# Performance work log

Hardware: AMD Instinct MI355X
Metric: run time of the kernel (lower is better)

## Reference

```python
import jax, jax.numpy as jnp
import numpy as np

B, T, D_IN = 8, 1024, 320
L, H, DK, DV, DM, DI = 6, 8, 64, 64, 512, 2048


def _pe_table():
    pos = np.arange(T, dtype=np.float32)[:, None]
    div = np.exp(np.arange(0, DM, 2, dtype=np.float32) * (-np.log(10000.0) / DM))
    pe = np.zeros((T, DM), np.float32)
    pe[:, 0::2] = np.sin(pos * div)
    pe[:, 1::2] = np.cos(pos * div)
    return jnp.asarray(pe)


def setup_inputs() -> dict:
    key = jax.random.key(0)
    ks = jax.random.split(key, 16)
    rn = lambda k, shape, std: (jax.random.normal(k, shape, jnp.float32) * std)
    inp = {}
    inp["padded_input"] = jax.random.normal(ks[0], (B, T, D_IN), jnp.float32)
    inp["input_lengths"] = jax.random.randint(ks[1], (B,), T // 2, T + 1)
    # input projection + input layernorm (weights stored as [in, out])
    inp["w_in"] = rn(ks[2], (D_IN, DM), 0.02)
    inp["b_in"] = jnp.zeros((DM,), jnp.float32)
    inp["ln_in_g"] = jnp.ones((DM,), jnp.float32)
    inp["ln_in_b"] = jnp.zeros((DM,), jnp.float32)
    inp["pe"] = _pe_table()
    # stacked per-layer params, leading dim L
    inp["wq"] = rn(ks[3], (L, DM, H * DK), np.sqrt(2.0 / (DM + DK)))
    inp["bq"] = jnp.zeros((L, H * DK), jnp.float32)
    inp["wk"] = rn(ks[4], (L, DM, H * DK), np.sqrt(2.0 / (DM + DK)))
    inp["bk"] = jnp.zeros((L, H * DK), jnp.float32)
    inp["wv"] = rn(ks[5], (L, DM, H * DV), np.sqrt(2.0 / (DM + DV)))
    inp["bv"] = jnp.zeros((L, H * DV), jnp.float32)
    inp["wfc"] = rn(ks[6], (L, H * DV, DM), np.sqrt(2.0 / (H * DV + DM)))
    inp["bfc"] = jnp.zeros((L, DM), jnp.float32)
    inp["ln1_g"] = jnp.ones((L, DM), jnp.float32)
    inp["ln1_b"] = jnp.zeros((L, DM), jnp.float32)
    inp["w1"] = rn(ks[7], (L, DM, DI), np.sqrt(2.0 / (DM + DI)))
    inp["b1"] = jnp.zeros((L, DI), jnp.float32)
    inp["w2"] = rn(ks[8], (L, DI, DM), np.sqrt(2.0 / (DM + DI)))
    inp["b2"] = jnp.zeros((L, DM), jnp.float32)
    inp["ln2_g"] = jnp.ones((L, DM), jnp.float32)
    inp["ln2_b"] = jnp.zeros((L, DM), jnp.float32)
    return inp


def _layer_norm(x, g, b):
    mu = jnp.mean(x, axis=-1, keepdims=True)
    var = jnp.var(x, axis=-1, keepdims=True)
    return (x - mu) * jax.lax.rsqrt(var + 1e-5) * g + b


def _encoder(padded_input, input_lengths, w_in, b_in, ln_in_g, ln_in_b, pe,
             wq, bq, wk, bk, wv, bv, wfc, bfc, ln1_g, ln1_b,
             w1, b1, w2, b2, ln2_g, ln2_b):
    pos = jnp.arange(T)
    key_pad = pos[None, :] >= input_lengths[:, None]          # [B,T] True at pad
    non_pad = (~key_pad).astype(padded_input.dtype)[:, :, None]  # [B,T,1]
    scale = 1.0 / jnp.sqrt(jnp.float32(DK))

    x = _layer_norm(padded_input @ w_in + b_in, ln_in_g, ln_in_b) + pe[None]

    def body(x, p):
        Wq, Bq, Wk, Bk, Wv, Bv, Wfc, Bfc, G1, Bn1, W1, Bf1, W2, Bf2, G2, Bn2 = p
        res = x
        q = (x @ Wq + Bq).reshape(B, T, H, DK)
        k = (x @ Wk + Bk).reshape(B, T, H, DK)
        v = (x @ Wv + Bv).reshape(B, T, H, DV)
        attn = jnp.einsum('bqhd,bkhd->bhqk', q, k) * scale
        attn = jnp.where(key_pad[:, None, None, :], -jnp.inf, attn)
        attn = jax.nn.softmax(attn, axis=-1)
        o = jnp.einsum('bhqk,bkhd->bqhd', attn, v).reshape(B, T, H * DV)
        x = _layer_norm(o @ Wfc + Bfc + res, G1, Bn1) * non_pad
        res = x
        h = jax.nn.relu(x @ W1 + Bf1)
        x = _layer_norm(h @ W2 + Bf2 + res, G2, Bn2) * non_pad
        return x, None

    x, _ = jax.lax.scan(body, x, (wq, bq, wk, bk, wv, bv, wfc, bfc,
                                  ln1_g, ln1_b, w1, b1, w2, b2, ln2_g, ln2_b))
    return x


def reference(padded_input, input_lengths, w_in, b_in, ln_in_g, ln_in_b, pe,
              wq, bq, wk, bk, wv, bv, wfc, bfc, ln1_g, ln1_b,
              w1, b1, w2, b2, ln2_g, ln2_b):
    # dropout is identity in eval mode
    return _encoder(padded_input, input_lengths, w_in, b_in, ln_in_g, ln_in_b, pe,
                    wq, bq, wk, bk, wv, bv, wfc, bfc, ln1_g, ln1_b,
                    w1, b1, w2, b2, ln2_g, ln2_b)
```

## Files before the change

### kernel.cpp

```cpp
#include <hip/hip_runtime.h>
#include <hip/hip_bf16.h>


typedef unsigned short bh16;
typedef __bf16 bf16x8 __attribute__((ext_vector_type(8)));
typedef float f32x4 __attribute__((ext_vector_type(4)));
typedef unsigned int u32x4 __attribute__((ext_vector_type(4)));
typedef unsigned int u32x2 __attribute__((ext_vector_type(2)));

#define DEVI static __device__ __forceinline__

DEVI bh16 f2bf(float f) {
  union { float f; unsigned u; } x; x.f = f;
  unsigned r = x.u + 0x7fffu + ((x.u >> 16) & 1u);
  return (bh16)(r >> 16);
}
DEVI float bf2f(bh16 u) {
  union { unsigned u; float f; } x; x.u = ((unsigned)u) << 16; return x.f;
}
DEVI bf16x8 ld16(const bh16* p) {
  return __builtin_bit_cast(bf16x8, *(const u32x4*)p);
}
DEVI bf16x8 ld16b(const char* p) {
  return __builtin_bit_cast(bf16x8, *(const u32x4*)p);
}
DEVI f32x4 mfma16(bf16x8 a, bf16x8 b, f32x4 c) {
  return __builtin_amdgcn_mfma_f32_16x16x32_bf16(a, b, c, 0, 0, 0);
}
DEVI void async16(const void* g, void* l) {
  __builtin_amdgcn_global_load_lds(
      (const __attribute__((address_space(1))) void*)g,
      (__attribute__((address_space(3))) void*)l, 16, 0, 0);
}

__global__ __launch_bounds__(256) void tcvt(
    const float* __restrict__ in, bh16* __restrict__ out,
    int K, int N, long long inLS, long long outLS, int rowOff) {
  int l = blockIdx.z;
  in += (size_t)l * inLS;
  out += (size_t)l * outLS + (size_t)rowOff * K;
  __shared__ float t[32][33];
  int n0 = blockIdx.x * 32, k0 = blockIdx.y * 32;
  int tx = threadIdx.x & 31, ty = threadIdx.x >> 5;
#pragma unroll
  for (int i = 0; i < 4; i++)
    t[ty + 8 * i][tx] = in[(size_t)(k0 + ty + 8 * i) * N + n0 + tx];
  __syncthreads();
#pragma unroll
  for (int i = 0; i < 4; i++)
    out[(size_t)(n0 + ty + 8 * i) * K + k0 + tx] = f2bf(t[tx][ty + 8 * i]);
}

__global__ __launch_bounds__(256) void bcat(
    const float* __restrict__ bq, const float* __restrict__ bk,
    const float* __restrict__ bv, float* __restrict__ out) {
  int l = blockIdx.x;
  for (int j = threadIdx.x; j < 1536; j += 256) {
    float v = (j < 512) ? bq[l * 512 + j]
            : (j < 1024) ? bk[l * 512 + j - 512] : bv[l * 512 + j - 1024];
    out[l * 1536 + j] = v;
  }
}

__global__ __launch_bounds__(256) void cvt_in(
    const float* __restrict__ in, bh16* __restrict__ out, int n4) {
  int i = blockIdx.x * 256 + threadIdx.x;
  if (i < n4) {
    float4 v = ((const float4*)in)[i];
    u32x2 pk;
    pk[0] = (unsigned)f2bf(v.x) | ((unsigned)f2bf(v.y) << 16);
    pk[1] = (unsigned)f2bf(v.z) | ((unsigned)f2bf(v.w) << 16);
    *(u32x2*)(out + (size_t)i * 4) = pk;
  }
}

template <int BM, int BN, int RELU, int OUTF32, int QKV>
__global__ __launch_bounds__(256) void gemm_bt(
    const bh16* __restrict__ A, const bh16* __restrict__ Bt,
    const float* __restrict__ bias, void* __restrict__ Cout,
    bh16* __restrict__ vtOut, int M, int N, int K) {
  constexpr int BK = 64;
  __shared__ __align__(16) bh16 As[2][BM * BK];
  __shared__ __align__(16) bh16 Bs[2][BN * BK];
  const int tid = threadIdx.x;
  const int wave = tid >> 6, lane = tid & 63;
  const int lq = lane & 15, grp = lane >> 4;
  const int p = blockIdx.x;
  const int xcd = p & 7, idx = p >> 3;
  const int m0 = (((xcd << 3) | (idx & 7))) * BM;
  const int n0 = (idx >> 3) * BN;
  constexpr int FM = BM / 32, FN = BN / 32;
  const int wr = wave >> 1, wc = wave & 1;
  f32x4 acc[FM][FN] = {};

  const int nk = K / BK;
  auto stage = [&](int buf, int kt) {
#pragma unroll
    for (int i = 0; i < BM / 32; ++i) {
      int off = i * 4096 + wave * 1024 + lane * 16;
      int row = off >> 7, col = off & 127;
      int sw = (row & 7) << 4;
      const char* g =
          (const char*)A + ((size_t)(m0 + row) * K + kt * BK) * 2 + (col ^ sw);
      async16(g, (char*)As[buf] + off);
    }
#pragma unroll
    for (int i = 0; i < BN / 32; ++i) {
      int off = i * 4096 + wave * 1024 + lane * 16;
      int row = off >> 7, col = off & 127;
      int sw = (row & 7) << 4;
      const char* g =
          (const char*)Bt + ((size_t)(n0 + row) * K + kt * BK) * 2 + (col ^ sw);
      async16(g, (char*)Bs[buf] + off);
    }
  };

  stage(0, 0);
  for (int kt = 0; kt < nk; ++kt) {
    int cur = kt & 1;
    __syncthreads();
    if (kt + 1 < nk) stage(cur ^ 1, kt + 1);
#pragma unroll
    for (int kk = 0; kk < 2; ++kk) {
      bf16x8 af[FM], bfr[FN];
#pragma unroll
      for (int i = 0; i < FM; ++i) {
        int row = wr * (BM / 2) + i * 16 + lq;
        int sw = (row & 7) << 4;
        af[i] = ld16b((char*)As[cur] + row * 128 + ((kk * 64 + grp * 16) ^ sw));
      }
#pragma unroll
      for (int j = 0; j < FN; ++j) {
        int row = wc * (BN / 2) + j * 16 + lq;
        int sw = (row & 7) << 4;
        bfr[j] = ld16b((char*)Bs[cur] + row * 128 + ((kk * 64 + grp * 16) ^ sw));
      }
#pragma unroll
      for (int i = 0; i < FM; ++i)
#pragma unroll
        for (int j = 0; j < FN; ++j)
          acc[i][j] = mfma16(af[i], bfr[j], acc[i][j]);
    }
  }
  if (QKV && n0 >= 1024) {
#pragma unroll
    for (int i = 0; i < FM; ++i) {
#pragma unroll
      for (int j = 0; j < FN; ++j) {
        int col = n0 + wc * (BN / 2) + j * 16 + lq;
        float bv = bias[col];
        int vc = col - 1024;
        int t0 = m0 + wr * (BM / 2) + i * 16 + grp * 4;
        int bb = t0 >> 10, tl = t0 & 1023;
        u32x2 pk;
        pk[0] = (unsigned)f2bf(acc[i][j][0] + bv) |
                ((unsigned)f2bf(acc[i][j][1] + bv) << 16);
        pk[1] = (unsigned)f2bf(acc[i][j][2] + bv) |
                ((unsigned)f2bf(acc[i][j][3] + bv) << 16);
        *(u32x2*)&vtOut[((size_t)(bb * 512 + vc)) * 1024 + tl] = pk;
      }
    }
    return;
  }
#pragma unroll
  for (int i = 0; i < FM; ++i) {
#pragma unroll
    for (int j = 0; j < FN; ++j) {
      int col = n0 + wc * (BN / 2) + j * 16 + lq;
      float bv = bias[col];
#pragma unroll
      for (int r = 0; r < 4; ++r) {
        int row = m0 + wr * (BM / 2) + i * 16 + grp * 4 + r;
        float v = acc[i][j][r] + bv;
        if (RELU) v = fmaxf(v, 0.f);
        if (OUTF32) ((float*)Cout)[(size_t)row * N + col] = v;
        else ((bh16*)Cout)[(size_t)row * N + col] = f2bf(v);
      }
    }
  }
}

__global__ __launch_bounds__(256) void ln_pe_k(
    const float* __restrict__ in, const float* __restrict__ g,
    const float* __restrict__ bta, const float* __restrict__ pe,
    float* __restrict__ xf, bh16* __restrict__ xb) {
  int wave = threadIdx.x >> 6, lane = threadIdx.x & 63;
  int row = blockIdx.x * 4 + wave;
  int t = row & 1023;
  const float* xr = in + (size_t)row * 512 + lane * 8;
  float4 a0 = ((const float4*)xr)[0], a1 = ((const float4*)xr)[1];
  float v[8] = {a0.x, a0.y, a0.z, a0.w, a1.x, a1.y, a1.z, a1.w};
  float s = 0.f, ss = 0.f;
#pragma unroll
  for (int j = 0; j < 8; j++) { s += v[j]; ss += v[j] * v[j]; }
#pragma unroll
  for (int m = 1; m < 64; m <<= 1) { s += __shfl_xor(s, m); ss += __shfl_xor(ss, m); }
  float mu = s * (1.f / 512.f);
  float rstd = rsqrtf(ss * (1.f / 512.f) - mu * mu + 1e-5f);
  int c0 = lane * 8;
  float o[8];
  u32x4 pk;
#pragma unroll
  for (int j = 0; j < 8; j++) {
    int c = c0 + j;
    o[j] = (v[j] - mu) * rstd * g[c] + bta[c] + pe[(size_t)t * 512 + c];
  }
  float4* xo = (float4*)(xf + (size_t)row * 512 + c0);
  xo[0] = make_float4(o[0], o[1], o[2], o[3]);
  xo[1] = make_float4(o[4], o[5], o[6], o[7]);
#pragma unroll
  for (int j = 0; j < 4; j++)
    pk[j] = (unsigned)f2bf(o[2 * j]) | ((unsigned)f2bf(o[2 * j + 1]) << 16);
  *(u32x4*)(xb + (size_t)row * 512 + c0) = pk;
}

__global__ __launch_bounds__(256) void ln_res_k(
    const bh16* __restrict__ gout, const float* __restrict__ res,
    const float* __restrict__ g, const float* __restrict__ bta,
    const int* __restrict__ lens,
    float* __restrict__ xf, bh16* __restrict__ xb) {
  int wave = threadIdx.x >> 6, lane = threadIdx.x & 63;
  int row = blockIdx.x * 4 + wave;
  int b = row >> 10, t = row & 1023;
  float nonpad = (t < lens[b]) ? 1.f : 0.f;
  int c0 = lane * 8;
  u32x4 graw = *(const u32x4*)(gout + (size_t)row * 512 + c0);
  const float* rr = res + (size_t)row * 512 + c0;
  float4 r0 = ((const float4*)rr)[0], r1 = ((const float4*)rr)[1];
  float v[8];
#pragma unroll
  for (int j = 0; j < 4; j++) {
    v[2 * j] = bf2f((bh16)(graw[j] & 0xffffu));
    v[2 * j + 1] = bf2f((bh16)(graw[j] >> 16));
  }
  v[0] += r0.x; v[1] += r0.y; v[2] += r0.z; v[3] += r0.w;
  v[4] += r1.x; v[5] += r1.y; v[6] += r1.z; v[7] += r1.w;
  float s = 0.f, ss = 0.f;
#pragma unroll
  for (int j = 0; j < 8; j++) { s += v[j]; ss += v[j] * v[j]; }
#pragma unroll
  for (int m = 1; m < 64; m <<= 1) { s += __shfl_xor(s, m); ss += __shfl_xor(ss, m); }
  float mu = s * (1.f / 512.f);
  float rstd = rsqrtf(ss * (1.f / 512.f) - mu * mu + 1e-5f);
  float o[8];
  u32x4 pk;
#pragma unroll
  for (int j = 0; j < 8; j++) {
    int c = c0 + j;
    o[j] = ((v[j] - mu) * rstd * g[c] + bta[c]) * nonpad;
  }
  float4* xo = (float4*)(xf + (size_t)row * 512 + c0);
  xo[0] = make_float4(o[0], o[1], o[2], o[3]);
  xo[1] = make_float4(o[4], o[5], o[6], o[7]);
#pragma unroll
  for (int j = 0; j < 4; j++)
    pk[j] = (unsigned)f2bf(o[2 * j]) | ((unsigned)f2bf(o[2 * j + 1]) << 16);
  *(u32x4*)(xb + (size_t)row * 512 + c0) = pk;
}

__global__ __launch_bounds__(512) void attn_k(
    const bh16* __restrict__ qkv, const bh16* __restrict__ vt,
    const int* __restrict__ lens, bh16* __restrict__ o) {
  constexpr int LDP = 72;
  __shared__ __align__(16) char Ks[2][8192];
  __shared__ __align__(16) char Vs[2][8192];
  __shared__ __align__(16) bh16 P[8][16 * LDP];
  int p = blockIdx.x;
  int xcd = p & 7, s = p >> 3;
  int bh = ((s & 7) << 3) | xcd;
  int qt = s >> 3;
  int b = bh >> 3, h = bh & 7;
  int len = lens[b];
  if (qt * 128 >= len) return;
  int tid = threadIdx.x;
  int wave = tid >> 6, lane = tid & 63;
  int lq = lane & 15, grp = lane >> 4;

  size_t qrow = (size_t)(b * 1024 + qt * 128 + wave * 16 + lq);
  const bh16* Qp = qkv + qrow * 1536 + h * 64;
  bf16x8 qf0 = ld16(Qp + grp * 8);
  bf16x8 qf1 = ld16(Qp + 32 + grp * 8);
  const char* Kbase = (const char*)(qkv + (size_t)(b * 1024) * 1536 + 512 + h * 64);
  const char* Vbase = (const char*)(vt + (size_t)(bh * 64) * 1024);
  bh16* Pw = P[wave];

  f32x4 oacc[4] = {};
  float m = -1e30f, lsum = 0.f;
  int nkb = (len + 63) >> 6;

  auto stage = [&](int buf, int kb) {
    int off = tid * 16;
    int row = off >> 7, cb = off & 127;
    int sw = (row & 7) << 4;
    async16(Kbase + (size_t)(kb * 64 + row) * 3072 + (cb ^ sw), Ks[buf] + off);
    async16(Vbase + (size_t)row * 2048 + kb * 128 + (cb ^ sw), Vs[buf] + off);
  };

  stage(0, 0);
  for (int kb = 0; kb < nkb; ++kb) {
    int cur = kb & 1;
    __syncthreads();
    if (kb + 1 < nkb) stage(cur ^ 1, kb + 1);
    int k64 = kb * 64;
    f32x4 st[4];
    __builtin_amdgcn_s_setprio(1);
#pragma unroll
    for (int sv = 0; sv < 4; ++sv) {
      int row = sv * 16 + lq, sw = (row & 7) << 4;
      const char* kp = Ks[cur] + row * 128;
      f32x4 z = {};
      z = mfma16(ld16b(kp + ((grp * 16) ^ sw)), qf0, z);
      z = mfma16(ld16b(kp + ((64 + grp * 16) ^ sw)), qf1, z);
      st[sv] = z;
    }
    __builtin_amdgcn_s_setprio(0);
    float tmax = -1e30f;
    if (k64 + 64 > len) {
#pragma unroll
      for (int sv = 0; sv < 4; ++sv)
#pragma unroll
        for (int r = 0; r < 4; ++r) {
          int key = k64 + sv * 16 + grp * 4 + r;
          float v = st[sv][r] * 0.125f;
          v = (key < len) ? v : -1e30f;
          st[sv][r] = v;
          tmax = fmaxf(tmax, v);
        }
    } else {
#pragma unroll
      for (int sv = 0; sv < 4; ++sv)
#pragma unroll
        for (int r = 0; r < 4; ++r) {
          float v = st[sv][r] * 0.125f;
          st[sv][r] = v;
          tmax = fmaxf(tmax, v);
        }
    }
    tmax = fmaxf(tmax, __shfl_xor(tmax, 16));
    tmax = fmaxf(tmax, __shfl_xor(tmax, 32));
    float newm = fmaxf(m, tmax);
    if (!__all(newm - m <= 8.f)) {
      float sc = __expf(m - newm);
      m = newm;
      lsum *= sc;
#pragma unroll
      for (int r = 0; r < 4; ++r) {
        float scr = __shfl(sc, grp * 4 + r);
#pragma unroll
        for (int dt = 0; dt < 4; ++dt) oacc[dt][r] *= scr;
      }
    }
    float rs = 0.f;
#pragma unroll
    for (int sv = 0; sv < 4; ++sv) {
      float p0 = __expf(st[sv][0] - m), p1 = __expf(st[sv][1] - m);
      float p2 = __expf(st[sv][2] - m), p3 = __expf(st[sv][3] - m);
      rs += (p0 + p1) + (p2 + p3);
      u32x2 pk;
      pk[0] = (unsigned)f2bf(p0) | ((unsigned)f2bf(p1) << 16);
      pk[1] = (unsigned)f2bf(p2) | ((unsigned)f2bf(p3) << 16);
      *(u32x2*)&Pw[lq * LDP + sv * 16 + grp * 4] = pk;
    }
    rs += __shfl_xor(rs, 16);
    rs += __shfl_xor(rs, 32);
    lsum += rs;
#pragma unroll
    for (int kk = 0; kk < 2; ++kk) {
      bf16x8 pa = ld16(Pw + lq * LDP + kk * 32 + grp * 8);
      __builtin_amdgcn_s_setprio(1);
#pragma unroll
      for (int dt = 0; dt < 4; ++dt) {
        int row = dt * 16 + lq, sw = (row & 7) << 4;
        bf16x8 vfr = ld16b(Vs[cur] + row * 128 + ((kk * 64 + grp * 16) ^ sw));
        oacc[dt] = mfma16(pa, vfr, oacc[dt]);
      }
      __builtin_amdgcn_s_setprio(0);
    }
  }
#pragma unroll
  for (int r = 0; r < 4; ++r) {
    float li = __shfl(lsum, grp * 4 + r);
    float inv = 1.f / li;
    int row = qt * 128 + wave * 16 + grp * 4 + r;
    bh16* orow = o + (size_t)(b * 1024 + row) * 512 + h * 64;
#pragma unroll
    for (int dt = 0; dt < 4; ++dt) orow[dt * 16 + lq] = f2bf(oacc[dt][r] * inv);
  }
}

extern "C" void kernel_launch(void* const* d_in, const int* in_sizes, int n_in,
                              void* d_out, int out_size, void* d_ws, size_t ws_size,
                              hipStream_t stream) {
  const float* padded = (const float*)d_in[0];
  const int* lens = (const int*)d_in[1];
  const float* w_in = (const float*)d_in[2];
  const float* b_in = (const float*)d_in[3];
  const float* ln_in_g = (const float*)d_in[4];
  const float* ln_in_b = (const float*)d_in[5];
  const float* pe = (const float*)d_in[6];
  const float* wq = (const float*)d_in[7];
  const float* bq = (const float*)d_in[8];
  const float* wk = (const float*)d_in[9];
  const float* bk = (const float*)d_in[10];
  const float* wv = (const float*)d_in[11];
  const float* bv = (const float*)d_in[12];
  const float* wfc = (const float*)d_in[13];
  const float* bfc = (const float*)d_in[14];
  const float* ln1_g = (const float*)d_in[15];
  const float* ln1_b = (const float*)d_in[16];
  const float* w1 = (const float*)d_in[17];
  const float* b1 = (const float*)d_in[18];
  const float* w2 = (const float*)d_in[19];
  const float* b2 = (const float*)d_in[20];
  const float* ln2_g = (const float*)d_in[21];
  const float* ln2_b = (const float*)d_in[22];

  char* ws = (char*)d_ws;
  size_t off = 0;
  auto alloc = [&](size_t bytes) -> char* {
    char* p = ws + off;
    off += (bytes + 255) & ~(size_t)255;
    return p;
  };
  bh16* WinT  = (bh16*)alloc((size_t)512 * 320 * 2);
  bh16* WqkvT = (bh16*)alloc((size_t)6 * 1536 * 512 * 2);
  bh16* WfcT  = (bh16*)alloc((size_t)6 * 512 * 512 * 2);
  bh16* W1T   = (bh16*)alloc((size_t)6 * 2048 * 512 * 2);
  bh16* W2T   = (bh16*)alloc((size_t)6 * 512 * 2048 * 2);
  float* bqkv = (float*)alloc((size_t)6 * 1536 * 4);
  bh16* xb    = (bh16*)alloc((size_t)8192 * 512 * 2);
  float* xf   = (float*)alloc((size_t)8192 * 512 * 4);
  bh16* qkvb  = (bh16*)alloc((size_t)8192 * 1536 * 2);
  bh16* vt    = (bh16*)alloc((size_t)64 * 64 * 1024 * 2);
  bh16* ob    = (bh16*)alloc((size_t)8192 * 512 * 2);
  float* tmp32 = (float*)alloc((size_t)8192 * 512 * 4);
  bh16* tmp16 = (bh16*)alloc((size_t)8192 * 512 * 2);
  bh16* hbuf  = (bh16*)alloc((size_t)8192 * 2048 * 2);
  bh16* padb  = hbuf;
  if (off > ws_size) return;

  tcvt<<<dim3(16, 10, 1), 256, 0, stream>>>(w_in, WinT, 320, 512, 0, 0, 0);
  tcvt<<<dim3(16, 16, 6), 256, 0, stream>>>(wq, WqkvT, 512, 512, 512 * 512, 1536 * 512, 0);
  tcvt<<<dim3(16, 16, 6), 256, 0, stream>>>(wk, WqkvT, 512, 512, 512 * 512, 1536 * 512, 512);
  tcvt<<<dim3(16, 16, 6), 256, 0, stream>>>(wv, WqkvT, 512, 512, 512 * 512, 1536 * 512, 1024);
  tcvt<<<dim3(16, 16, 6), 256, 0, stream>>>(wfc, WfcT, 512, 512, 512 * 512, 512 * 512, 0);
  tcvt<<<dim3(64, 16, 6), 256, 0, stream>>>(w1, W1T, 512, 2048, (long long)512 * 2048, (long long)2048 * 512, 0);
  tcvt<<<dim3(16, 64, 6), 256, 0, stream>>>(w2, W2T, 2048, 512, (long long)2048 * 512, (long long)512 * 2048, 0);
  bcat<<<6, 256, 0, stream>>>(bq, bk, bv, bqkv);
  cvt_in<<<2560, 256, 0, stream>>>(padded, padb, 655360);

  gemm_bt<128, 64, 0, 1, 0><<<512, 256, 0, stream>>>(
      padb, WinT, b_in, tmp32, nullptr, 8192, 512, 320);
  ln_pe_k<<<2048, 256, 0, stream>>>(tmp32, ln_in_g, ln_in_b, pe, xf, xb);

  for (int l = 0; l < 6; ++l) {
    gemm_bt<128, 128, 0, 0, 1><<<768, 256, 0, stream>>>(
        xb, WqkvT + (size_t)l * 1536 * 512, bqkv + l * 1536, qkvb, vt,
        8192, 1536, 512);
    attn_k<<<512, 512, 0, stream>>>(qkvb, vt, lens, ob);
    gemm_bt<128, 64, 0, 0, 0><<<512, 256, 0, stream>>>(
        ob, WfcT + (size_t)l * 512 * 512, bfc + l * 512, tmp16, nullptr,
        8192, 512, 512);
    ln_res_k<<<2048, 256, 0, stream>>>(tmp16, xf, ln1_g + l * 512, ln1_b + l * 512,
                                       lens, xf, xb);
    gemm_bt<128, 128, 1, 0, 0><<<1024, 256, 0, stream>>>(
        xb, W1T + (size_t)l * 2048 * 512, b1 + l * 2048, hbuf, nullptr,
        8192, 2048, 512);
    gemm_bt<128, 64, 0, 0, 0><<<512, 256, 0, stream>>>(
        hbuf, W2T + (size_t)l * 512 * 2048, b2 + l * 512, tmp16, nullptr,
        8192, 512, 2048);
    float* xfo = (l == 5) ? (float*)d_out : xf;
    ln_res_k<<<2048, 256, 0, stream>>>(tmp16, xf, ln2_g + l * 512, ln2_b + l * 512,
                                       lens, xfo, xb);
  }
}
```

Baseline: 859.1 us.

## Triple-buffer GEMM loads, fix tile at 128x64, keep residual in bf16

The GEMM now uses a three-stage LDS pipeline with a partial vmcnt wait and raw barrier instead of double buffering with __syncthreads. It also raises MFMA priority and fixes every GEMM at 128x64 tiles, which doubles the grid for the QKV and FFN1 launches. Separately, the fp32 residual stream is dropped: layer norms read and write only the bf16 activation, and fp32 is written only for the final output. This cuts memory traffic but adds bf16 rounding to the residual path, which may reduce accuracy.

```diff
diff --git a/kernel.cpp b/kernel.cpp
--- a/kernel.cpp
+++ b/kernel.cpp
@@ -74,14 +74,14 @@
   }
 }
 
-template <int BM, int BN, int RELU, int OUTF32, int QKV>
+template <int RELU, int OUTF32, int QKV>
 __global__ __launch_bounds__(256) void gemm_bt(
     const bh16* __restrict__ A, const bh16* __restrict__ Bt,
     const float* __restrict__ bias, void* __restrict__ Cout,
     bh16* __restrict__ vtOut, int M, int N, int K) {
-  constexpr int BK = 64;
-  __shared__ __align__(16) bh16 As[2][BM * BK];
-  __shared__ __align__(16) bh16 Bs[2][BN * BK];
+  constexpr int BM = 128, BN = 64, BK = 64;
+  __shared__ __align__(16) bh16 As[3][BM * BK];
+  __shared__ __align__(16) bh16 Bs[3][BN * BK];
   const int tid = threadIdx.x;
   const int wave = tid >> 6, lane = tid & 63;
   const int lq = lane & 15, grp = lane >> 4;
@@ -116,10 +116,13 @@
   };
 
   stage(0, 0);
+  stage(1, 1);
+  int cur = 0, nxt = 2;
   for (int kt = 0; kt < nk; ++kt) {
-    int cur = kt & 1;
-    __syncthreads();
-    if (kt + 1 < nk) stage(cur ^ 1, kt + 1);
+    asm volatile("s_waitcnt vmcnt(6)" ::: "memory");
+    __builtin_amdgcn_s_barrier();
+    __builtin_amdgcn_sched_barrier(0);
+    if (kt + 2 < nk) stage(nxt, kt + 2);
 #pragma unroll
     for (int kk = 0; kk < 2; ++kk) {
       bf16x8 af[FM], bfr[FN];
@@ -135,12 +138,16 @@
         int sw = (row & 7) << 4;
         bfr[j] = ld16b((char*)Bs[cur] + row * 128 + ((kk * 64 + grp * 16) ^ sw));
       }
+      __builtin_amdgcn_s_setprio(1);
 #pragma unroll
       for (int i = 0; i < FM; ++i)
 #pragma unroll
         for (int j = 0; j < FN; ++j)
           acc[i][j] = mfma16(af[i], bfr[j], acc[i][j]);
-    }
+      __builtin_amdgcn_s_setprio(0);
+    }
+    cur = (cur == 2) ? 0 : cur + 1;
+    nxt = (nxt == 2) ? 0 : nxt + 1;
   }
   if (QKV && n0 >= 1024) {
 #pragma unroll
@@ -183,7 +190,7 @@
 __global__ __launch_bounds__(256) void ln_pe_k(
     const float* __restrict__ in, const float* __restrict__ g,
     const float* __restrict__ bta, const float* __restrict__ pe,
-    float* __restrict__ xf, bh16* __restrict__ xb) {
+    bh16* __restrict__ xb) {
   int wave = threadIdx.x >> 6, lane = threadIdx.x & 63;
   int row = blockIdx.x * 4 + wave;
   int t = row & 1023;
@@ -205,9 +212,6 @@
     int c = c0 + j;
     o[j] = (v[j] - mu) * rstd * g[c] + bta[c] + pe[(size_t)t * 512 + c];
   }
-  float4* xo = (float4*)(xf + (size_t)row * 512 + c0);
-  xo[0] = make_float4(o[0], o[1], o[2], o[3]);
-  xo[1] = make_float4(o[4], o[5], o[6], o[7]);
 #pragma unroll
   for (int j = 0; j < 4; j++)
     pk[j] = (unsigned)f2bf(o[2 * j]) | ((unsigned)f2bf(o[2 * j + 1]) << 16);
@@ -215,26 +219,22 @@
 }
 
 __global__ __launch_bounds__(256) void ln_res_k(
-    const bh16* __restrict__ gout, const float* __restrict__ res,
+    const bh16* __restrict__ gout, const bh16* res,
     const float* __restrict__ g, const float* __restrict__ bta,
-    const int* __restrict__ lens,
-    float* __restrict__ xf, bh16* __restrict__ xb) {
+    const int* __restrict__ lens, bh16* xb, float* fout) {
   int wave = threadIdx.x >> 6, lane = threadIdx.x & 63;
   int row = blockIdx.x * 4 + wave;
   int b = row >> 10, t = row & 1023;
   float nonpad = (t < lens[b]) ? 1.f : 0.f;
   int c0 = lane * 8;
   u32x4 graw = *(const u32x4*)(gout + (size_t)row * 512 + c0);
-  const float* rr = res + (size_t)row * 512 + c0;
-  float4 r0 = ((const float4*)rr)[0], r1 = ((const float4*)rr)[1];
+  u32x4 rraw = *(const u32x4*)(res + (size_t)row * 512 + c0);
   float v[8];
 #pragma unroll
   for (int j = 0; j < 4; j++) {
-    v[2 * j] = bf2f((bh16)(graw[j] & 0xffffu));
-    v[2 * j + 1] = bf2f((bh16)(graw[j] >> 16));
-  }
-  v[0] += r0.x; v[1] += r0.y; v[2] += r0.z; v[3] += r0.w;
-  v[4] += r1.x; v[5] += r1.y; v[6] += r1.z; v[7] += r1.w;
+    v[2 * j] = bf2f((bh16)(graw[j] & 0xffffu)) + bf2f((bh16)(rraw[j] & 0xffffu));
+    v[2 * j + 1] = bf2f((bh16)(graw[j] >> 16)) + bf2f((bh16)(rraw[j] >> 16));
+  }
   float s = 0.f, ss = 0.f;
 #pragma unroll
   for (int j = 0; j < 8; j++) { s += v[j]; ss += v[j] * v[j]; }
@@ -249,13 +249,15 @@
     int c = c0 + j;
     o[j] = ((v[j] - mu) * rstd * g[c] + bta[c]) * nonpad;
   }
-  float4* xo = (float4*)(xf + (size_t)row * 512 + c0);
-  xo[0] = make_float4(o[0], o[1], o[2], o[3]);
-  xo[1] = make_float4(o[4], o[5], o[6], o[7]);
 #pragma unroll
   for (int j = 0; j < 4; j++)
     pk[j] = (unsigned)f2bf(o[2 * j]) | ((unsigned)f2bf(o[2 * j + 1]) << 16);
   *(u32x4*)(xb + (size_t)row * 512 + c0) = pk;
+  if (fout) {
+    float4* xo = (float4*)(fout + (size_t)row * 512 + c0);
+    xo[0] = make_float4(o[0], o[1], o[2], o[3]);
+    xo[1] = make_float4(o[4], o[5], o[6], o[7]);
+  }
 }
 
 __global__ __launch_bounds__(512) void attn_k(
@@ -429,7 +431,6 @@
   bh16* W2T   = (bh16*)alloc((size_t)6 * 512 * 2048 * 2);
   float* bqkv = (float*)alloc((size_t)6 * 1536 * 4);
   bh16* xb    = (bh16*)alloc((size_t)8192 * 512 * 2);
-  float* xf   = (float*)alloc((size_t)8192 * 512 * 4);
   bh16* qkvb  = (bh16*)alloc((size_t)8192 * 1536 * 2);
   bh16* vt    = (bh16*)alloc((size_t)64 * 64 * 1024 * 2);
   bh16* ob    = (bh16*)alloc((size_t)8192 * 512 * 2);
@@ -449,28 +450,27 @@
   bcat<<<6, 256, 0, stream>>>(bq, bk, bv, bqkv);
   cvt_in<<<2560, 256, 0, stream>>>(padded, padb, 655360);
 
-  gemm_bt<128, 64, 0, 1, 0><<<512, 256, 0, stream>>>(
+  gemm_bt<0, 1, 0><<<512, 256, 0, stream>>>(
       padb, WinT, b_in, tmp32, nullptr, 8192, 512, 320);
-  ln_pe_k<<<2048, 256, 0, stream>>>(tmp32, ln_in_g, ln_in_b, pe, xf, xb);
+  ln_pe_k<<<2048, 256, 0, stream>>>(tmp32, ln_in_g, ln_in_b, pe, xb);
 
   for (int l = 0; l < 6; ++l) {
-    gemm_bt<128, 128, 0, 0, 1><<<768, 256, 0, stream>>>(
+    gemm_bt<0, 0, 1><<<1536, 256, 0, stream>>>(
         xb, WqkvT + (size_t)l * 1536 * 512, bqkv + l * 1536, qkvb, vt,
         8192, 1536, 512);
     attn_k<<<512, 512, 0, stream>>>(qkvb, vt, lens, ob);
-    gemm_bt<128, 64, 0, 0, 0><<<512, 256, 0, stream>>>(
+    gemm_bt<0, 0, 0><<<512, 256, 0, stream>>>(
         ob, WfcT + (size_t)l * 512 * 512, bfc + l * 512, tmp16, nullptr,
         8192, 512, 512);
-    ln_res_k<<<2048, 256, 0, stream>>>(tmp16, xf, ln1_g + l * 512, ln1_b + l * 512,
-                                       lens, xf, xb);
-    gemm_bt<128, 128, 1, 0, 0><<<1024, 256, 0, stream>>>(
+    ln_res_k<<<2048, 256, 0, stream>>>(tmp16, xb, ln1_g + l * 512, ln1_b + l * 512,
+                                       lens, xb, nullptr);
+    gemm_bt<1, 0, 0><<<2048, 256, 0, stream>>>(
         xb, W1T + (size_t)l * 2048 * 512, b1 + l * 2048, hbuf, nullptr,
         8192, 2048, 512);
-    gemm_bt<128, 64, 0, 0, 0><<<512, 256, 0, stream>>>(
+    gemm_bt<0, 0, 0><<<512, 256, 0, stream>>>(
         hbuf, W2T + (size_t)l * 512 * 2048, b2 + l * 512, tmp16, nullptr,
         8192, 512, 2048);
-    float* xfo = (l == 5) ? (float*)d_out : xf;
-    ln_res_k<<<2048, 256, 0, stream>>>(tmp16, xf, ln2_g + l * 512, ln2_b + l * 512,
-                                       lens, xfo, xb);
-  }
-}
+    ln_res_k<<<2048, 256, 0, stream>>>(tmp16, xb, ln2_g + l * 512, ln2_b + l * 512,
+                                       lens, xb, (l == 5) ? (float*)d_out : nullptr);
+  }
+}
```

Result: no change. 869.8 us (+1.3%).
